# Kernel optimization log

Hardware: AMD Instinct MI355X
Metric: run time of the kernel (lower is better)

The kernel has to match this reference:

```python
import jax, jax.numpy as jnp
import numpy as np


def setup_inputs() -> dict:
    key = jax.random.key(0)
    k1, k2, k3 = jax.random.split(key, 3)
    B, T, D = 8, 2048, 128      # *A = (B, T), address_size = D
    N, V = 4096, 512            # num_addresses, *B = (V,)
    return {
        "selector": jax.random.normal(k1, (B, T, D), dtype=jnp.float32),
        "param_bank": jax.random.normal(k2, (N, V), dtype=jnp.float32),
        "address_space": jax.random.normal(k3, (N, D), dtype=jnp.float32),
    }


def reference(selector, param_bank, address_space):
    # scores: [B, T, N] = selector @ address_space^T (unscaled)
    scores = jnp.einsum("btd,nd->btn", selector, address_space)
    weights = jax.nn.softmax(scores, axis=-1)
    # weighted sum over the bank: [B, T, V]
    return jnp.einsum("btn,nv->btv", weights, param_bank)
```

## Files before the change

kernel.cpp:

```cpp
#include <hip/hip_runtime.h>

typedef __attribute__((ext_vector_type(8))) short bf16x8;
typedef __attribute__((ext_vector_type(8))) _Float16 f16x8;
typedef __attribute__((ext_vector_type(2))) __fp16 fp16v2;
typedef __attribute__((ext_vector_type(16))) float f32x16;

#define DDIM 128
#define NADDR 4096
#define VDIM 512
#define MTOT 16384
#define NT 32
#define NTILES (NADDR/NT)
#define LOG2E 1.44269504088896340736f

__device__ __forceinline__ unsigned pkhi(float hi, float lo){
  return __builtin_amdgcn_perm(__float_as_uint(hi), __float_as_uint(lo), 0x07060302u);
}

__global__ __launch_bounds__(512)
void prep_k(const float* __restrict__ addr, _Float16* __restrict__ kt)
{
  const int nt = blockIdx.x, ts = threadIdx.x;
  const int ks = ts >> 6, r = (ts >> 1) & 31, hh = ts & 1;
  const float* s = addr + (size_t)(nt*NT + r)*DDIM + 16*ks + 8*hh;
  float4 a = *(const float4*)s;
  float4 b = *(const float4*)(s + 4);
  union { f16x8 v; fp16v2 h[4]; } u;
  u.h[0] = __builtin_amdgcn_cvt_pkrtz(a.x, a.y);
  u.h[1] = __builtin_amdgcn_cvt_pkrtz(a.z, a.w);
  u.h[2] = __builtin_amdgcn_cvt_pkrtz(b.x, b.y);
  u.h[3] = __builtin_amdgcn_cvt_pkrtz(b.z, b.w);
  ((f16x8*)kt)[(size_t)nt*512 + ts] = u.v;
}

__global__ __launch_bounds__(1024)
void prep_v(const float* __restrict__ bank, short* __restrict__ vt)
{
  const int nt = blockIdx.x, t = threadIdx.x;
  const int vv = t & 511, half = t >> 9;
  const float* src = bank + (size_t)(nt*NT + half*16) * VDIM + vv;
  float v[16];
  #pragma unroll
  for (int k = 0; k < 16; ++k) v[k] = src[(size_t)k * VDIM];
  uint4 p0, p1;
  p0.x = pkhi(v[1],  v[0]);  p0.y = pkhi(v[3],  v[2]);
  p0.z = pkhi(v[5],  v[4]);  p0.w = pkhi(v[7],  v[6]);
  p1.x = pkhi(v[9],  v[8]);  p1.y = pkhi(v[11], v[10]);
  p1.z = pkhi(v[13], v[12]); p1.w = pkhi(v[15], v[14]);
  uint4* dst = (uint4*)vt + ((size_t)nt*1024 + t)*2;
  dst[0] = p0; dst[1] = p1;
}

__global__ __launch_bounds__(256, 4)
void pass1_kernel(const float* __restrict__ sel,
                  const _Float16* __restrict__ kt,
                  short* __restrict__ pt,
                  float* __restrict__ den,
                  int m_off)
{
  const int tid  = threadIdx.x;
  const int wave = tid >> 6;
  const int lane = tid & 63;
  const int h    = lane >> 5;
  const int c32  = lane & 31;

  const int nq  = blockIdx.x & 7;
  const int mbl = blockIdx.x >> 3;
  const int m0  = m_off + mbl * 128;
  const int wm  = wave * 32;
  const int mtl = mbl * 4 + wave;

  f16x8 aQ[8];
  {
    const float* q = sel + (size_t)(m0 + wm + c32) * DDIM + 8*h;
    #pragma unroll
    for (int ks = 0; ks < 8; ++ks){
      float4 a = *(const float4*)(q + 16*ks);
      float4 b = *(const float4*)(q + 16*ks + 4);
      f16x8 f;
      f[0]=(_Float16)(a.x*LOG2E); f[1]=(_Float16)(a.y*LOG2E);
      f[2]=(_Float16)(a.z*LOG2E); f[3]=(_Float16)(a.w*LOG2E);
      f[4]=(_Float16)(b.x*LOG2E); f[5]=(_Float16)(b.y*LOG2E);
      f[6]=(_Float16)(b.z*LOG2E); f[7]=(_Float16)(b.w*LOG2E);
      aQ[ks] = f;
    }
  }

  f32x16 zc;
  #pragma unroll
  for (int r=0;r<16;++r) zc[r] = 0.f;
  asm volatile("" : "+v"(zc));

  float lacc = 0.f;

  const f16x8* kb = (const f16x8*)kt + (size_t)(nq*16)*512;
  bf16x8* pbase = (bf16x8*)pt + (size_t)mtl * NTILES * 128;
  const int fl = c32*2 + h;

  for (int t = 0; t < 16; ++t){
    f16x8 aK[8];
    #pragma unroll
    for (int ks=0;ks<8;++ks)
      aK[ks] = kb[(size_t)t*512 + ks*64 + fl];

    __builtin_amdgcn_s_setprio(1);
    f32x16 sAcc0, sAcc1;
    sAcc0 = __builtin_amdgcn_mfma_f32_32x32x16_f16(aK[0], aQ[0], zc, 0,0,0);
    sAcc1 = __builtin_amdgcn_mfma_f32_32x32x16_f16(aK[1], aQ[1], zc, 0,0,0);
    #pragma unroll
    for (int ks=1; ks<4; ++ks){
      sAcc0 = __builtin_amdgcn_mfma_f32_32x32x16_f16(aK[2*ks],   aQ[2*ks],   sAcc0, 0,0,0);
      sAcc1 = __builtin_amdgcn_mfma_f32_32x32x16_f16(aK[2*ks+1], aQ[2*ks+1], sAcc1, 0,0,0);
    }
    __builtin_amdgcn_s_setprio(0);

    unsigned dw[2][4];
    #pragma unroll
    for (int j=0;j<2;++j)
      #pragma unroll
      for (int i=0;i<4;++i){
        float pa = __builtin_amdgcn_exp2f(sAcc0[8*j + 2*i]     + sAcc1[8*j + 2*i]);
        float pb = __builtin_amdgcn_exp2f(sAcc0[8*j + 2*i + 1] + sAcc1[8*j + 2*i + 1]);
        lacc += __uint_as_float(__float_as_uint(pa) & 0xffff0000u);
        lacc += __uint_as_float(__float_as_uint(pb) & 0xffff0000u);
        dw[j][i] = pkhi(pb, pa);
      }

    const int nt = nq*16 + t;
    #pragma unroll
    for (int j=0;j<2;++j){
      auto s02 = __builtin_amdgcn_permlane32_swap(dw[j][0], dw[j][2], false, false);
      auto s13 = __builtin_amdgcn_permlane32_swap(dw[j][1], dw[j][3], false, false);
      union { unsigned u[4]; bf16x8 v; } ap;
      ap.u[0] = s02[0]; ap.u[1] = s13[0]; ap.u[2] = s02[1]; ap.u[3] = s13[1];
      pbase[((size_t)nt*64 + lane)*2 + j] = ap.v;
    }
  }

  float tot = lacc + __shfl_xor(lacc, 32);
  if (lane < 32)
    den[(size_t)(m0 + wm + c32)*8 + nq] = tot;
}

__global__ __launch_bounds__(512, 2)
void pass2_kernel(const short* __restrict__ pt,
                  const short* __restrict__ vt,
                  const float* __restrict__ den,
                  float* __restrict__ out,
                  int m_off)
{
  const int tid  = threadIdx.x;
  const int wave = tid >> 6;
  const int lane = tid & 63;
  const int h    = lane >> 5;
  const int c32  = lane & 31;

  const int mtl = blockIdx.x;
  const int v0  = wave * 64;
  const int mg  = m_off + mtl * 32;

  const bf16x8* pa = (const bf16x8*)pt + (size_t)mtl * NTILES * 128;
  const bf16x8* vb = (const bf16x8*)vt;

  f32x16 oAcc[2];
  #pragma unroll
  for (int jv=0;jv<2;++jv)
    #pragma unroll
    for (int r=0;r<16;++r) oAcc[jv][r] = 0.f;

  bf16x8 A0a, A1a, B00a, B01a, B10a, B11a;
  bf16x8 A0b, A1b, B00b, B01b, B10b, B11b;

#define P2L(NTI, A0, A1, B00, B01, B10, B11)                              \
  { const size_t o = (size_t)(NTI);                                       \
    A0  = pa[(o*64 + lane)*2];                                            \
    A1  = pa[(o*64 + lane)*2 + 1];                                        \
    B00 = vb[o*2048 + (size_t)(      v0      + c32)*2 + h];               \
    B01 = vb[o*2048 + (size_t)(      v0 + 32 + c32)*2 + h];               \
    B10 = vb[o*2048 + (size_t)(512 + v0      + c32)*2 + h];               \
    B11 = vb[o*2048 + (size_t)(512 + v0 + 32 + c32)*2 + h]; }

#define P2M(A0, A1, B00, B01, B10, B11)                                   \
  { oAcc[0] = __builtin_amdgcn_mfma_f32_32x32x16_bf16(A0, B00, oAcc[0], 0,0,0); \
    oAcc[1] = __builtin_amdgcn_mfma_f32_32x32x16_bf16(A0, B01, oAcc[1], 0,0,0); \
    oAcc[0] = __builtin_amdgcn_mfma_f32_32x32x16_bf16(A1, B10, oAcc[0], 0,0,0); \
    oAcc[1] = __builtin_amdgcn_mfma_f32_32x32x16_bf16(A1, B11, oAcc[1], 0,0,0); }

  P2L(0, A0a, A1a, B00a, B01a, B10a, B11a);
  for (int nt = 0; nt < NTILES; nt += 2){
    P2L(nt+1, A0b, A1b, B00b, B01b, B10b, B11b);
    P2M(A0a, A1a, B00a, B01a, B10a, B11a);
    if (nt + 2 < NTILES) P2L(nt+2, A0a, A1a, B00a, B01a, B10a, B11a);
    P2M(A0b, A1b, B00b, B01b, B10b, B11b);
  }
#undef P2L
#undef P2M

  #pragma unroll
  for (int r=0;r<16;++r){
    const int mrow = (r&3) + 8*(r>>2) + 4*h;
    const int m = mg + mrow;
    float4 d0 = *(const float4*)&den[(size_t)m*8];
    float4 d1 = *(const float4*)&den[(size_t)m*8 + 4];
    const float inv = 1.0f / (d0.x+d0.y+d0.z+d0.w + d1.x+d1.y+d1.z+d1.w);
    float* op = out + (size_t)m * VDIM + v0 + c32;
    op[0]  = oAcc[0][r] * inv;
    op[32] = oAcc[1][r] * inv;
  }
}

extern "C" void kernel_launch(void* const* d_in, const int* in_sizes, int n_in,
                              void* d_out, int out_size, void* d_ws, size_t ws_size,
                              hipStream_t stream) {
  const float* sel  = (const float*)d_in[0];
  const float* bank = (const float*)d_in[1];
  const float* addr = (const float*)d_in[2];
  float* out = (float*)d_out;

  char* ws = (char*)d_ws;
  _Float16* kt  = (_Float16*)ws;
  short*    vt  = (short*)(ws + (1u<<20));
  float*    den = (float*)(ws + (5u<<20));
  short*    pt  = (short*)(ws + (6u<<20));

  int CM = MTOT;
  while (CM > 2048 && (size_t)(6u<<20) + (size_t)CM*NADDR*2 > ws_size) CM >>= 1;

  hipLaunchKernelGGL(prep_k, dim3(NTILES), dim3(512),  0, stream, addr, kt);
  hipLaunchKernelGGL(prep_v, dim3(NTILES), dim3(1024), 0, stream, bank, vt);
  for (int mo = 0; mo < MTOT; mo += CM){
    hipLaunchKernelGGL(pass1_kernel, dim3(CM/16), dim3(256), 0, stream,
                       sel, kt, pt, den, mo);
    hipLaunchKernelGGL(pass2_kernel, dim3(CM/32), dim3(512), 0, stream,
                       pt, vt, den, out, mo);
  }
}
```

Measured before the change: 234.5 us.

## Process two M-tiles per pass2 block with async LDS-staged P loads

Pass2 now gives each block two 32-row M tiles, so every V fragment loaded from global memory feeds twice as many MFMAs and V traffic is halved. P tiles are streamed into a per-wave 4-slot LDS ring with global_load_lds and a fixed vmcnt wait, while V fragments are double-buffered in registers. The grid is halved and launch bounds are relaxed for pass1 and pass2. The cost is 128KB of LDS per block, fewer blocks in flight, and a hand-tuned waitcnt that depends on exact instruction counts.

Result: faster. 204.2 us (-12.9%).

```diff
diff --git a/kernel.cpp b/kernel.cpp
--- a/kernel.cpp
+++ b/kernel.cpp
@@ -16,6 +16,11 @@
 __device__ __forceinline__ unsigned pkhi(float hi, float lo){
   return __builtin_amdgcn_perm(__float_as_uint(hi), __float_as_uint(lo), 0x07060302u);
 }
+
+#define GLD_LDS(GSRC, LDST)                                                     \
+  __builtin_amdgcn_global_load_lds(                                             \
+      (const __attribute__((address_space(1))) unsigned*)(GSRC),                \
+      (__attribute__((address_space(3))) unsigned*)(LDST), 16, 0, 0)
 
 __global__ __launch_bounds__(512)
 void prep_k(const float* __restrict__ addr, _Float16* __restrict__ kt)
@@ -51,7 +56,7 @@
   dst[0] = p0; dst[1] = p1;
 }
 
-__global__ __launch_bounds__(256, 4)
+__global__ __launch_bounds__(256, 3)
 void pass1_kernel(const float* __restrict__ sel,
                   const _Float16* __restrict__ kt,
                   short* __restrict__ pt,
@@ -142,70 +147,99 @@
     den[(size_t)(m0 + wm + c32)*8 + nq] = tot;
 }
 
-__global__ __launch_bounds__(512, 2)
+__global__ __launch_bounds__(512)
 void pass2_kernel(const short* __restrict__ pt,
                   const short* __restrict__ vt,
                   const float* __restrict__ den,
                   float* __restrict__ out,
                   int m_off)
 {
+  __shared__ __align__(16) short sA[8][4][2048];
+
   const int tid  = threadIdx.x;
   const int wave = tid >> 6;
   const int lane = tid & 63;
   const int h    = lane >> 5;
   const int c32  = lane & 31;
-
-  const int mtl = blockIdx.x;
-  const int v0  = wave * 64;
-  const int mg  = m_off + mtl * 32;
-
-  const bf16x8* pa = (const bf16x8*)pt + (size_t)mtl * NTILES * 128;
+  const int v0   = wave * 64;
+
+  const int mtl0 = blockIdx.x * 2;
+  const int mg   = m_off + mtl0 * 32;
+
+  const char* pA0 = (const char*)pt + (size_t)mtl0 * NTILES * 2048 + (size_t)lane*32;
+  const char* pA1 = pA0 + (size_t)NTILES * 2048;
   const bf16x8* vb = (const bf16x8*)vt;
 
-  f32x16 oAcc[2];
-  #pragma unroll
-  for (int jv=0;jv<2;++jv)
-    #pragma unroll
-    for (int r=0;r<16;++r) oAcc[jv][r] = 0.f;
-
-  bf16x8 A0a, A1a, B00a, B01a, B10a, B11a;
-  bf16x8 A0b, A1b, B00b, B01b, B10b, B11b;
-
-#define P2L(NTI, A0, A1, B00, B01, B10, B11)                              \
-  { const size_t o = (size_t)(NTI);                                       \
-    A0  = pa[(o*64 + lane)*2];                                            \
-    A1  = pa[(o*64 + lane)*2 + 1];                                        \
-    B00 = vb[o*2048 + (size_t)(      v0      + c32)*2 + h];               \
-    B01 = vb[o*2048 + (size_t)(      v0 + 32 + c32)*2 + h];               \
-    B10 = vb[o*2048 + (size_t)(512 + v0      + c32)*2 + h];               \
-    B11 = vb[o*2048 + (size_t)(512 + v0 + 32 + c32)*2 + h]; }
-
-#define P2M(A0, A1, B00, B01, B10, B11)                                   \
-  { oAcc[0] = __builtin_amdgcn_mfma_f32_32x32x16_bf16(A0, B00, oAcc[0], 0,0,0); \
-    oAcc[1] = __builtin_amdgcn_mfma_f32_32x32x16_bf16(A0, B01, oAcc[1], 0,0,0); \
-    oAcc[0] = __builtin_amdgcn_mfma_f32_32x32x16_bf16(A1, B10, oAcc[0], 0,0,0); \
-    oAcc[1] = __builtin_amdgcn_mfma_f32_32x32x16_bf16(A1, B11, oAcc[1], 0,0,0); }
-
-  P2L(0, A0a, A1a, B00a, B01a, B10a, B11a);
-  for (int nt = 0; nt < NTILES; nt += 2){
-    P2L(nt+1, A0b, A1b, B00b, B01b, B10b, B11b);
-    P2M(A0a, A1a, B00a, B01a, B10a, B11a);
-    if (nt + 2 < NTILES) P2L(nt+2, A0a, A1a, B00a, B01a, B10a, B11a);
-    P2M(A0b, A1b, B00b, B01b, B10b, B11b);
-  }
-#undef P2L
-#undef P2M
-
-  #pragma unroll
-  for (int r=0;r<16;++r){
-    const int mrow = (r&3) + 8*(r>>2) + 4*h;
-    const int m = mg + mrow;
-    float4 d0 = *(const float4*)&den[(size_t)m*8];
-    float4 d1 = *(const float4*)&den[(size_t)m*8 + 4];
-    const float inv = 1.0f / (d0.x+d0.y+d0.z+d0.w + d1.x+d1.y+d1.z+d1.w);
-    float* op = out + (size_t)m * VDIM + v0 + c32;
-    op[0]  = oAcc[0][r] * inv;
-    op[32] = oAcc[1][r] * inv;
+  short* sw = &sA[wave][0][0];
+
+  f32x16 oAcc[2][2];
+  #pragma unroll
+  for (int mt=0;mt<2;++mt)
+    #pragma unroll
+    for (int vg=0;vg<2;++vg)
+      #pragma unroll
+      for (int r=0;r<16;++r) oAcc[mt][vg][r] = 0.f;
+
+  bf16x8 Br[2][4];
+
+#define ISSUE_A(TL, SL) {                                                     \
+    const size_t tb = (size_t)(TL)*2048;                                      \
+    GLD_LDS(pA0 + tb,      sw + (SL)*2048);                                   \
+    GLD_LDS(pA0 + tb + 16, sw + (SL)*2048 + 512);                             \
+    GLD_LDS(pA1 + tb,      sw + (SL)*2048 + 1024);                            \
+    GLD_LDS(pA1 + tb + 16, sw + (SL)*2048 + 1536); }
+
+#define LOAD_B(TL, RI) { const size_t o2 = (size_t)(TL)*2048;                 \
+    Br[RI][0] = vb[o2 + (size_t)(      v0      + c32)*2 + h];                 \
+    Br[RI][1] = vb[o2 + (size_t)(      v0 + 32 + c32)*2 + h];                 \
+    Br[RI][2] = vb[o2 + (size_t)(512 + v0      + c32)*2 + h];                 \
+    Br[RI][3] = vb[o2 + (size_t)(512 + v0 + 32 + c32)*2 + h]; }
+
+  ISSUE_A(0, 0); ISSUE_A(1, 1); ISSUE_A(2, 2);
+  LOAD_B(0, 0);  LOAD_B(1, 1);
+
+  for (int p = 0; p < NTILES; ++p){
+    const int bi = p & 1;
+    ISSUE_A((p+3) & (NTILES-1), (p+3) & 3);
+
+    asm volatile("s_waitcnt vmcnt(20)" ::: "memory");
+
+    bf16x8 aA[2][2];
+    #pragma unroll
+    for (int mt=0;mt<2;++mt)
+      #pragma unroll
+      for (int j=0;j<2;++j)
+        aA[mt][j] = *(const bf16x8*)(sw + (size_t)(p&3)*2048 + (mt*2+j)*512 + lane*8);
+
+    __builtin_amdgcn_s_setprio(1);
+    #pragma unroll
+    for (int mt=0;mt<2;++mt)
+      #pragma unroll
+      for (int vg=0;vg<2;++vg){
+        oAcc[mt][vg] = __builtin_amdgcn_mfma_f32_32x32x16_bf16(aA[mt][0], Br[bi][vg],   oAcc[mt][vg], 0,0,0);
+        oAcc[mt][vg] = __builtin_amdgcn_mfma_f32_32x32x16_bf16(aA[mt][1], Br[bi][2+vg], oAcc[mt][vg], 0,0,0);
+      }
+    __builtin_amdgcn_s_setprio(0);
+
+    LOAD_B((p+2) & (NTILES-1), bi);
+  }
+#undef ISSUE_A
+#undef LOAD_B
+
+  #pragma unroll
+  for (int mt=0;mt<2;++mt){
+    const int mbase = mg + mt*32;
+    #pragma unroll
+    for (int r=0;r<16;++r){
+      const int mrow = (r&3) + 8*(r>>2) + 4*h;
+      const int m = mbase + mrow;
+      float4 d0 = *(const float4*)&den[(size_t)m*8];
+      float4 d1 = *(const float4*)&den[(size_t)m*8 + 4];
+      const float inv = 1.0f / (d0.x+d0.y+d0.z+d0.w + d1.x+d1.y+d1.z+d1.w);
+      float* op = out + (size_t)m * VDIM + v0 + c32;
+      op[0]  = oAcc[mt][0][r] * inv;
+      op[32] = oAcc[mt][1][r] * inv;
+    }
   }
 }
 
@@ -231,7 +265,7 @@
   for (int mo = 0; mo < MTOT; mo += CM){
     hipLaunchKernelGGL(pass1_kernel, dim3(CM/16), dim3(256), 0, stream,
                        sel, kt, pt, den, mo);
-    hipLaunchKernelGGL(pass2_kernel, dim3(CM/32), dim3(512), 0, stream,
+    hipLaunchKernelGGL(pass2_kernel, dim3(CM/64), dim3(512), 0, stream,
                        pt, vt, den, out, mo);
   }
 }
```

## Stage P tiles through LDS and share across 16-wave pass2 blocks

Applied to the files above, without the earlier changes.

Pass2 now uses 1024-thread blocks, each covering two 32-row M tiles. Every wave owns 32 V columns and reads the P fragments from a four-slot LDS ring buffer, so P is loaded from global once per block instead of once per wave. The pass1 store layout changes to match the new LDS staging order, and pass1 occupancy drops to 3 blocks per CU. In exchange, every tile step now needs a block-wide barrier across 16 waves, and each wave's V-operand reuse is halved.

Result: faster. 195.0 us (-16.9%).

```diff
diff --git a/kernel.cpp b/kernel.cpp
--- a/kernel.cpp
+++ b/kernel.cpp
@@ -51,7 +51,7 @@
   dst[0] = p0; dst[1] = p1;
 }
 
-__global__ __launch_bounds__(256, 4)
+__global__ __launch_bounds__(256, 3)
 void pass1_kernel(const float* __restrict__ sel,
                   const _Float16* __restrict__ kt,
                   short* __restrict__ pt,
@@ -133,7 +133,7 @@
       auto s13 = __builtin_amdgcn_permlane32_swap(dw[j][1], dw[j][3], false, false);
       union { unsigned u[4]; bf16x8 v; } ap;
       ap.u[0] = s02[0]; ap.u[1] = s13[0]; ap.u[2] = s02[1]; ap.u[3] = s13[1];
-      pbase[((size_t)nt*64 + lane)*2 + j] = ap.v;
+      pbase[(size_t)nt*128 + j*64 + lane] = ap.v;
     }
   }
 
@@ -142,70 +142,97 @@
     den[(size_t)(m0 + wm + c32)*8 + nq] = tot;
 }
 
-__global__ __launch_bounds__(512, 2)
+__global__ __launch_bounds__(1024, 4)
 void pass2_kernel(const short* __restrict__ pt,
                   const short* __restrict__ vt,
                   const float* __restrict__ den,
                   float* __restrict__ out,
                   int m_off)
 {
+  __shared__ __align__(16) short sA[4][2048];
+
   const int tid  = threadIdx.x;
   const int wave = tid >> 6;
   const int lane = tid & 63;
   const int h    = lane >> 5;
   const int c32  = lane & 31;
-
-  const int mtl = blockIdx.x;
-  const int v0  = wave * 64;
-  const int mg  = m_off + mtl * 32;
-
-  const bf16x8* pa = (const bf16x8*)pt + (size_t)mtl * NTILES * 128;
+  const int v0   = wave * 32;
+
+  const int mtl0 = blockIdx.x * 2;
+  const int mg   = m_off + mtl0 * 32;
+
   const bf16x8* vb = (const bf16x8*)vt;
 
-  f32x16 oAcc[2];
-  #pragma unroll
-  for (int jv=0;jv<2;++jv)
-    #pragma unroll
-    for (int r=0;r<16;++r) oAcc[jv][r] = 0.f;
-
-  bf16x8 A0a, A1a, B00a, B01a, B10a, B11a;
-  bf16x8 A0b, A1b, B00b, B01b, B10b, B11b;
-
-#define P2L(NTI, A0, A1, B00, B01, B10, B11)                              \
-  { const size_t o = (size_t)(NTI);                                       \
-    A0  = pa[(o*64 + lane)*2];                                            \
-    A1  = pa[(o*64 + lane)*2 + 1];                                        \
-    B00 = vb[o*2048 + (size_t)(      v0      + c32)*2 + h];               \
-    B01 = vb[o*2048 + (size_t)(      v0 + 32 + c32)*2 + h];               \
-    B10 = vb[o*2048 + (size_t)(512 + v0      + c32)*2 + h];               \
-    B11 = vb[o*2048 + (size_t)(512 + v0 + 32 + c32)*2 + h]; }
-
-#define P2M(A0, A1, B00, B01, B10, B11)                                   \
-  { oAcc[0] = __builtin_amdgcn_mfma_f32_32x32x16_bf16(A0, B00, oAcc[0], 0,0,0); \
-    oAcc[1] = __builtin_amdgcn_mfma_f32_32x32x16_bf16(A0, B01, oAcc[1], 0,0,0); \
-    oAcc[0] = __builtin_amdgcn_mfma_f32_32x32x16_bf16(A1, B10, oAcc[0], 0,0,0); \
-    oAcc[1] = __builtin_amdgcn_mfma_f32_32x32x16_bf16(A1, B11, oAcc[1], 0,0,0); }
-
-  P2L(0, A0a, A1a, B00a, B01a, B10a, B11a);
-  for (int nt = 0; nt < NTILES; nt += 2){
-    P2L(nt+1, A0b, A1b, B00b, B01b, B10b, B11b);
-    P2M(A0a, A1a, B00a, B01a, B10a, B11a);
-    if (nt + 2 < NTILES) P2L(nt+2, A0a, A1a, B00a, B01a, B10a, B11a);
-    P2M(A0b, A1b, B00b, B01b, B10b, B11b);
-  }
-#undef P2L
-#undef P2M
-
-  #pragma unroll
-  for (int r=0;r<16;++r){
-    const int mrow = (r&3) + 8*(r>>2) + 4*h;
-    const int m = mg + mrow;
-    float4 d0 = *(const float4*)&den[(size_t)m*8];
-    float4 d1 = *(const float4*)&den[(size_t)m*8 + 4];
-    const float inv = 1.0f / (d0.x+d0.y+d0.z+d0.w + d1.x+d1.y+d1.z+d1.w);
-    float* op = out + (size_t)m * VDIM + v0 + c32;
-    op[0]  = oAcc[0][r] * inv;
-    op[32] = oAcc[1][r] * inv;
+  const int f  = tid >> 8;
+  const int lw = (tid >> 2) & 63;
+  const int bw = (tid & 3) * 4;
+  const char* psrc = (const char*)pt
+      + (size_t)(mtl0 + (f >> 1)) * NTILES * 2048
+      + (size_t)(f & 1) * 1024 + (size_t)lw * 16 + bw;
+  unsigned* sdw = (unsigned*)&sA[0][0];
+
+  f32x16 oAcc0, oAcc1;
+  #pragma unroll
+  for (int r=0;r<16;++r){ oAcc0[r] = 0.f; oAcc1[r] = 0.f; }
+
+  bf16x8 BrA0, BrA1, BrB0, BrB1;
+  unsigned dwA, dwB;
+
+#define LOAD_B(TL, R0, R1) { const size_t o2 = (size_t)((TL)&(NTILES-1))*2048; \
+    R0 = vb[o2 + (size_t)(      v0 + c32)*2 + h];                              \
+    R1 = vb[o2 + (size_t)(512 + v0 + c32)*2 + h]; }
+
+  {
+    unsigned d0 = *(const unsigned*)(psrc);
+    unsigned d1 = *(const unsigned*)(psrc + 2048);
+    dwA = *(const unsigned*)(psrc + 2*2048);
+    dwB = *(const unsigned*)(psrc + 3*2048);
+    LOAD_B(0, BrA0, BrA1);
+    LOAD_B(1, BrB0, BrB1);
+    sdw[tid] = d0;
+    sdw[1024 + tid] = d1;
+    __syncthreads();
+  }
+
+#define BODY(P, DW, B0, B1) {                                                  \
+    sdw[((((P)+2)&3)<<10) + tid] = DW;                   \
+    const short* sb = &sA[0][0] + (((P)&3)<<11);                               \
+    bf16x8 a0 = *(const bf16x8*)(sb +        lane*8);                          \
+    bf16x8 a1 = *(const bf16x8*)(sb +  512 + lane*8);                          \
+    bf16x8 a2 = *(const bf16x8*)(sb + 1024 + lane*8);                          \
+    bf16x8 a3 = *(const bf16x8*)(sb + 1536 + lane*8);                          \
+    __builtin_amdgcn_s_setprio(1);                                             \
+    oAcc0 = __builtin_amdgcn_mfma_f32_32x32x16_bf16(a0, B0, oAcc0, 0,0,0);     \
+    oAcc1 = __builtin_amdgcn_mfma_f32_32x32x16_bf16(a2, B0, oAcc1, 0,0,0);     \
+    oAcc0 = __builtin_amdgcn_mfma_f32_32x32x16_bf16(a1, B1, oAcc0, 0,0,0);     \
+    oAcc1 = __builtin_amdgcn_mfma_f32_32x32x16_bf16(a3, B1, oAcc1, 0,0,0);     \
+    __builtin_amdgcn_s_setprio(0);                                             \
+    LOAD_B((P)+2, B0, B1);                                                     \
+    DW = *(const unsigned*)(psrc + (size_t)(((P)+4)&(NTILES-1))*2048);         \
+    asm volatile("s_waitcnt lgkmcnt(0)" ::: "memory");                         \
+    __builtin_amdgcn_s_barrier();                                              \
+    asm volatile("" ::: "memory"); }
+
+  for (int p = 0; p < NTILES; p += 2){
+    BODY(p,   dwA, BrA0, BrA1);
+    BODY(p+1, dwB, BrB0, BrB1);
+  }
+#undef BODY
+#undef LOAD_B
+
+  #pragma unroll
+  for (int mt=0; mt<2; ++mt){
+    const f32x16& oa = mt ? oAcc1 : oAcc0;
+    const int mbase = mg + mt*32;
+    #pragma unroll
+    for (int r=0;r<16;++r){
+      const int mrow = (r&3) + 8*(r>>2) + 4*h;
+      const int m = mbase + mrow;
+      float4 d0 = *(const float4*)&den[(size_t)m*8];
+      float4 d1 = *(const float4*)&den[(size_t)m*8 + 4];
+      const float inv = 1.0f / (d0.x+d0.y+d0.z+d0.w + d1.x+d1.y+d1.z+d1.w);
+      out[(size_t)m * VDIM + v0 + c32] = oa[r] * inv;
+    }
   }
 }
 
@@ -231,7 +258,7 @@
   for (int mo = 0; mo < MTOT; mo += CM){
     hipLaunchKernelGGL(pass1_kernel, dim3(CM/16), dim3(256), 0, stream,
                        sel, kt, pt, den, mo);
-    hipLaunchKernelGGL(pass2_kernel, dim3(CM/32), dim3(512), 0, stream,
+    hipLaunchKernelGGL(pass2_kernel, dim3(CM/64), dim3(1024), 0, stream,
                        pt, vt, den, out, mo);
   }
 }
```
